# Optimization experiments

Measured on AMD Instinct MI355X. Metric: run time of the kernel, lower is better.

Reference implementation:

```python
import jax, jax.numpy as jnp
import numpy as np

EPS = 1e-5

def layernorm(x, w, b):
    mu = jnp.mean(x, axis=-1, keepdims=True)
    var = jnp.mean((x - mu) ** 2, axis=-1, keepdims=True)
    return (x - mu) / jnp.sqrt(var + EPS) * w + b

def setup_inputs() -> dict:
    key = jax.random.key(0)
    ks = jax.random.split(key, 20)
    N, E, G = 50000, 800000, 512
    IN, OUT, TXT, MAN = 128, 128, 768, 14
    d = {
        "x": jax.random.normal(ks[0], (N, IN), jnp.float32),
        "edge_index": jax.random.randint(ks[1], (2, E), 0, N),
        "batch": jnp.sort(jax.random.randint(ks[2], (N,), 0, G)),
        "batch_size": G,
        "text_embedding": jax.random.normal(ks[3], (G, TXT), jnp.float32),
        "features_embedding": jax.random.normal(ks[4], (G, MAN), jnp.float32),
        # params
        "ln_proj_w": jnp.ones((IN,)), "ln_proj_b": jnp.zeros((IN,)),
        "W_l": jax.random.normal(ks[5], (IN, OUT)) / np.sqrt(IN),
        "b_l": jnp.zeros((OUT,)),
        "W_r": jax.random.normal(ks[6], (IN, OUT)) / np.sqrt(IN),
        "ln_conv_w": jnp.ones((OUT,)), "ln_conv_b": jnp.zeros((OUT,)),
        "gate_w": jax.random.normal(ks[7], (OUT, 1)) / np.sqrt(OUT),
        "gate_b": jnp.zeros((1,)),
        "graph_weight": jnp.asarray(1.0, jnp.float32),
        "msg_W": jax.random.normal(ks[8], (TXT, OUT)) / np.sqrt(TXT),
        "msg_b": jnp.zeros((OUT,)),
        "feat_W": jax.random.normal(ks[9], (MAN, OUT)) / np.sqrt(MAN),
        "feat_b": jnp.zeros((OUT,)),
        "mixed_w": jnp.ones((3 * OUT,)), "mixed_b": jnp.zeros((3 * OUT,)),
        "fc1_W": jax.random.normal(ks[10], (3 * OUT, 1)) / np.sqrt(3 * OUT),
        "fc1_b": jnp.zeros((1,)),
    }
    return d

def reference(x, edge_index, batch, batch_size, text_embedding, features_embedding,
              ln_proj_w, ln_proj_b, W_l, b_l, W_r, ln_conv_w, ln_conv_b,
              gate_w, gate_b, graph_weight, msg_W, msg_b, feat_W, feat_b,
              mixed_w, mixed_b, fc1_W, fc1_b):
    N = x.shape[0]
    src, dst = edge_index[0], edge_index[1]
    # project_norm
    h = layernorm(x, ln_proj_w, ln_proj_b)
    # GraphSAGE (SAGEConv, mean aggregation): out = mean_j(h_j) @ W_l + b + h @ W_r
    msgs = h[src]                                   # [E, IN] gather
    agg = jax.ops.segment_sum(msgs, dst, num_segments=N)
    deg = jax.ops.segment_sum(jnp.ones((src.shape[0],), h.dtype), dst, num_segments=N)
    mean_nb = agg / jnp.maximum(deg, 1.0)[:, None]
    h = mean_nb @ W_l + b_l + h @ W_r
    # layernorm + gelu (HomogeneousGraphConvolution)
    h = jax.nn.gelu(layernorm(h, ln_conv_w, ln_conv_b), approximate=False)
    # AttentionalAggregation: scatter-softmax over `batch`
    gate = (h @ gate_w + gate_b)[:, 0]              # [N]
    seg_max = jax.ops.segment_max(gate, batch, num_segments=batch_size)
    seg_max = jnp.where(jnp.isfinite(seg_max), seg_max, 0.0)
    e = jnp.exp(gate - seg_max[batch])
    denom = jax.ops.segment_sum(e, batch, num_segments=batch_size)
    attn = (e / denom[batch])[:, None]              # [N,1]
    graph_embedding = jax.ops.segment_sum(attn * h, batch, num_segments=batch_size)
    # dropout is identity in eval mode
    weighted = graph_weight * graph_embedding
    msg_emb = jax.nn.gelu(text_embedding @ msg_W + msg_b, approximate=False)
    feat_emb = jax.nn.gelu(features_embedding @ feat_W + feat_b, approximate=False)
    emb = jnp.concatenate([weighted, msg_emb, feat_emb], axis=1)
    emb = layernorm(emb, mixed_w, mixed_b)
    logits = emb @ fc1_W + fc1_b
    return (logits, graph_embedding, attn)
```

## Files before the change

kernel.cpp:

```cpp
#include <hip/hip_runtime.h>


typedef unsigned short ushort_t;
typedef __attribute__((ext_vector_type(8))) short bf16x8;
typedef __attribute__((ext_vector_type(4))) float floatx4;

__device__ __forceinline__ float b2f(ushort_t u) {
    union { unsigned int i; float f; } v; v.i = ((unsigned int)u) << 16; return v.f;
}
__device__ __forceinline__ ushort_t f2b(float f) {
    union { float f; unsigned int i; } v; v.f = f;
    unsigned int x = v.i;
    return (ushort_t)((x + 0x7FFFu + ((x >> 16) & 1u)) >> 16);
}
__device__ __forceinline__ float gelu_f(float x) {
    return 0.5f * x * (1.0f + erff(x * 0.70710678118654752440f));
}
__device__ __forceinline__ float waveReduceSum(float v) {
#pragma unroll
    for (int o = 32; o; o >>= 1) v += __shfl_xor(v, o, 64);
    return v;
}
__device__ __forceinline__ int waveReduceSumI(int v) {
#pragma unroll
    for (int o = 32; o; o >>= 1) v += __shfl_xor(v, o, 64);
    return v;
}
__device__ __forceinline__ float waveReduceMax(float v) {
#pragma unroll
    for (int o = 32; o; o >>= 1) v = fmaxf(v, __shfl_xor(v, o, 64));
    return v;
}
__device__ __forceinline__ int lowerBound(const int* __restrict__ a, int n, int v) {
    int lo = 0, hi = n;
    while (lo < hi) { int mid = (lo + hi) >> 1; if (a[mid] < v) lo = mid + 1; else hi = mid; }
    return lo;
}

__global__ void __launch_bounds__(256) k_prepln(
    const float* __restrict__ x, const float* __restrict__ w, const float* __restrict__ b,
    const float* __restrict__ Wl, const float* __restrict__ Wr,
    ushort_t* __restrict__ Wt, ushort_t* __restrict__ hb, int* __restrict__ deg, int N) {
    int bid = blockIdx.x;
    if (bid < 128) {
        int id = bid * 256 + threadIdx.x;
        int n = id >> 8, k = id & 255;
        float v = (k < 128) ? Wl[k * 128 + n] : Wr[(k - 128) * 128 + n];
        Wt[n * 256 + k] = f2b(v);
        return;
    }
    int lb = bid - 128;
    if (threadIdx.x < 4) {
        int rz = lb * 4 + threadIdx.x;
        if (rz < N) deg[rz] = 0;
    }
    int row  = lb * 4 + (threadIdx.x >> 6);
    int lane = threadIdx.x & 63;
    if (row >= N) return;
    size_t base = (size_t)row * 128;
    float2 xv = ((const float2*)(x + base))[lane];
    float v0 = xv.x, v1 = xv.y;
    float s  = waveReduceSum(v0 + v1);
    float s2 = waveReduceSum(v0 * v0 + v1 * v1);
    float mu = s * (1.0f / 128.0f);
    float var = s2 * (1.0f / 128.0f) - mu * mu;
    float rstd = 1.0f / sqrtf(var + 1e-5f);
    int d = lane * 2;
    ushort2 ov;
    ov.x = f2b((v0 - mu) * rstd * w[d]     + b[d]);
    ov.y = f2b((v1 - mu) * rstd * w[d + 1] + b[d + 1]);
    ((ushort2*)(hb + base))[lane] = ov;
}

__global__ void __launch_bounds__(256) k_count(
    const int* __restrict__ ei, int* __restrict__ deg, int E) {
    int i0 = (blockIdx.x * 256 + threadIdx.x) * 4;
    const int* dstp = ei + E;
    if (i0 + 3 < E) {
        int4 d4 = *(const int4*)(dstp + i0);
        atomicAdd(&deg[d4.x], 1);
        atomicAdd(&deg[d4.y], 1);
        atomicAdd(&deg[d4.z], 1);
        atomicAdd(&deg[d4.w], 1);
    } else {
        int e1 = min(i0 + 4, E);
        for (int i = i0; i < e1; i++) atomicAdd(&deg[dstp[i]], 1);
    }
}

__global__ void __launch_bounds__(256) k_cursor3(
    const int* __restrict__ deg, int* __restrict__ cursor, int* __restrict__ wcur, int N) {
    int c = blockIdx.x, t = threadIdx.x;
    __shared__ int sb[256];
    __shared__ int cw[4];
    int lim = c << 8;
    int part = 0;
    for (int j = t; j < lim; j += 256) part += deg[j];
    part = waveReduceSumI(part);
    int lane = t & 63, wv = t >> 6;
    if (lane == 0) cw[wv] = part;
    int i = (c << 8) + t;
    int v = (i < N) ? deg[i] : 0;
    sb[t] = v;
    __syncthreads();
    for (int o = 1; o < 256; o <<= 1) {
        int a = (t >= o) ? sb[t - o] : 0;
        __syncthreads();
        sb[t] += a;
        __syncthreads();
    }
    int coff = cw[0] + cw[1] + cw[2] + cw[3];
    if (i < N) {
        int cv = sb[t] - v + coff;
        cursor[i] = cv;
        wcur[i]   = cv;
    }
}

__global__ void __launch_bounds__(256) k_place(
    const int* __restrict__ ei, int* __restrict__ wcur, int* __restrict__ nbr, int E) {
    int i0 = (blockIdx.x * 256 + threadIdx.x) * 4;
    if (i0 + 3 < E) {
        int4 s4 = *(const int4*)(ei + i0);
        int4 d4 = *(const int4*)(ei + E + i0);
        nbr[atomicAdd(&wcur[d4.x], 1)] = s4.x;
        nbr[atomicAdd(&wcur[d4.y], 1)] = s4.y;
        nbr[atomicAdd(&wcur[d4.z], 1)] = s4.z;
        nbr[atomicAdd(&wcur[d4.w], 1)] = s4.w;
    } else {
        int e1 = min(i0 + 4, E);
        for (int i = i0; i < e1; i++) {
            int s = ei[i], d = ei[E + i];
            nbr[atomicAdd(&wcur[d], 1)] = s;
        }
    }
}

__global__ void __launch_bounds__(256) k_aggemm(
    const ushort_t* __restrict__ hb, const ushort_t* __restrict__ Wt,
    const float* __restrict__ bl, const float* __restrict__ lnw,
    const float* __restrict__ lnb, const float* __restrict__ gw,
    const float* __restrict__ gb, const int* __restrict__ deg,
    const int* __restrict__ cursor, const int* __restrict__ nbr,
    ushort_t* __restrict__ h3b, float* __restrict__ gate, int N) {
    __shared__ ushort_t A[16][264];
    __shared__ float H2[16][132];
    int t = threadIdx.x;
    int row0 = blockIdx.x * 16;
    int w = t >> 6, l = t & 63;
    int sub = l >> 4, li = l & 15;
    for (int rr = 0; rr < 4; rr++) {
        int r = w * 4 + rr;
        int node = row0 + r; if (node >= N) node = N - 1;
        if (sub == 2) {
            bf16x8 hv = *(const bf16x8*)(hb + (size_t)node * 128 + li * 8);
            *(bf16x8*)&A[r][128 + li * 8] = hv;
        }
        int dg = deg[node];
        int st = cursor[node];
        float a0 = 0.f, a1 = 0.f, a2 = 0.f, a3 = 0.f;
        float a4 = 0.f, a5 = 0.f, a6 = 0.f, a7 = 0.f;
        for (int j = 0; j < dg; j += 8) {
            int i0 = j + sub, i1 = j + 4 + sub;
            bf16x8 r0 = {0,0,0,0,0,0,0,0};
            bf16x8 r1 = {0,0,0,0,0,0,0,0};
            if (i0 < dg) {
                int s = nbr[st + i0];
                r0 = *(const bf16x8*)(hb + (size_t)s * 128 + li * 8);
            }
            if (i1 < dg) {
                int s = nbr[st + i1];
                r1 = *(const bf16x8*)(hb + (size_t)s * 128 + li * 8);
            }
            a0 += b2f((ushort_t)r0[0]) + b2f((ushort_t)r1[0]);
            a1 += b2f((ushort_t)r0[1]) + b2f((ushort_t)r1[1]);
            a2 += b2f((ushort_t)r0[2]) + b2f((ushort_t)r1[2]);
            a3 += b2f((ushort_t)r0[3]) + b2f((ushort_t)r1[3]);
            a4 += b2f((ushort_t)r0[4]) + b2f((ushort_t)r1[4]);
            a5 += b2f((ushort_t)r0[5]) + b2f((ushort_t)r1[5]);
            a6 += b2f((ushort_t)r0[6]) + b2f((ushort_t)r1[6]);
            a7 += b2f((ushort_t)r0[7]) + b2f((ushort_t)r1[7]);
        }
        a0 += __shfl_xor(a0, 16, 64); a0 += __shfl_xor(a0, 32, 64);
        a1 += __shfl_xor(a1, 16, 64); a1 += __shfl_xor(a1, 32, 64);
        a2 += __shfl_xor(a2, 16, 64); a2 += __shfl_xor(a2, 32, 64);
        a3 += __shfl_xor(a3, 16, 64); a3 += __shfl_xor(a3, 32, 64);
        a4 += __shfl_xor(a4, 16, 64); a4 += __shfl_xor(a4, 32, 64);
        a5 += __shfl_xor(a5, 16, 64); a5 += __shfl_xor(a5, 32, 64);
        a6 += __shfl_xor(a6, 16, 64); a6 += __shfl_xor(a6, 32, 64);
        a7 += __shfl_xor(a7, 16, 64); a7 += __shfl_xor(a7, 32, 64);
        if (sub == 0) {
            float inv = 1.0f / fmaxf((float)dg, 1.0f);
            bf16x8 ov;
            ov[0] = (short)f2b(a0 * inv); ov[1] = (short)f2b(a1 * inv);
            ov[2] = (short)f2b(a2 * inv); ov[3] = (short)f2b(a3 * inv);
            ov[4] = (short)f2b(a4 * inv); ov[5] = (short)f2b(a5 * inv);
            ov[6] = (short)f2b(a6 * inv); ov[7] = (short)f2b(a7 * inv);
            *(bf16x8*)&A[r][li * 8] = ov;
        }
    }
    __syncthreads();
    int m16 = l & 15, quad = l >> 4;
    int n0 = w * 32 + m16;
    int n1 = n0 + 16;
    floatx4 acc0 = {0.f, 0.f, 0.f, 0.f}, acc1 = {0.f, 0.f, 0.f, 0.f};
    for (int ks = 0; ks < 256; ks += 32) {
        bf16x8 a  = *(const bf16x8*)&A[m16][ks + quad * 8];
        bf16x8 b0 = *(const bf16x8*)(Wt + (size_t)n0 * 256 + ks + quad * 8);
        bf16x8 b1 = *(const bf16x8*)(Wt + (size_t)n1 * 256 + ks + quad * 8);
        acc0 = __builtin_amdgcn_mfma_f32_16x16x32_bf16(a, b0, acc0, 0, 0, 0);
        acc1 = __builtin_amdgcn_mfma_f32_16x16x32_bf16(a, b1, acc1, 0, 0, 0);
    }
#pragma unroll
    for (int i = 0; i < 4; i++) {
        H2[quad * 4 + i][n0] = acc0[i];
        H2[quad * 4 + i][n1] = acc1[i];
    }
    __syncthreads();
    int d = l * 2;
    float bb0 = bl[d],  bb1 = bl[d + 1];
    float lw0 = lnw[d], lw1 = lnw[d + 1];
    float lb0 = lnb[d], lb1 = lnb[d + 1];
    float gw0 = gw[d],  gw1 = gw[d + 1];
    float gbias = gb[0];
#pragma unroll
    for (int rr = 0; rr < 4; rr++) {
        int r = w * 4 + rr;
        int row = row0 + r;
        if (row >= N) break;
        float v0 = H2[r][d] + bb0, v1 = H2[r][d + 1] + bb1;
        float s  = waveReduceSum(v0 + v1);
        float s2 = waveReduceSum(v0 * v0 + v1 * v1);
        float mu = s * (1.f / 128.f);
        float var = s2 * (1.f / 128.f) - mu * mu;
        float rstd = 1.0f / sqrtf(var + 1e-5f);
        float g0 = gelu_f((v0 - mu) * rstd * lw0 + lb0);
        float g1 = gelu_f((v1 - mu) * rstd * lw1 + lb1);
        float gp = waveReduceSum(g0 * gw0 + g1 * gw1);
        ushort2 ov; ov.x = f2b(g0); ov.y = f2b(g1);
        ((ushort2*)(h3b + (size_t)row * 128))[l] = ov;
        if (l == 0) gate[row] = gp + gbias;
    }
}

__global__ void __launch_bounds__(128) k_attntail(
    const float* __restrict__ gate, const ushort_t* __restrict__ h3b,
    const int* __restrict__ batch,
    const float* __restrict__ text, const float* __restrict__ feats,
    const float* __restrict__ msgW, const float* __restrict__ msgb,
    const float* __restrict__ featW, const float* __restrict__ featb,
    const float* __restrict__ gwt, const float* __restrict__ mixw,
    const float* __restrict__ mixb, const float* __restrict__ fc1W,
    const float* __restrict__ fc1b,
    float* __restrict__ ge_out, float* __restrict__ attn_out,
    float* __restrict__ logits, int N, int G) {
    int g = blockIdx.x, t = threadIdx.x;
    __shared__ int sbound[2];
    __shared__ float wbuf[2];
    __shared__ float pbuf[128];
    __shared__ float txt[768];
    __shared__ float rbuf[4];
    if (t < 2) sbound[t] = lowerBound(batch, N, g + t);
    for (int i = t; i < 768; i += 128) txt[i] = text[(size_t)g * 768 + i];
    __syncthreads();
    int s0 = sbound[0], s1 = sbound[1];
    int lane = t & 63, wv = t >> 6;
    float acc = 0.f;
    if (s1 > s0) {
        float m = -3.0e38f;
        for (int i = s0 + t; i < s1; i += 128) m = fmaxf(m, gate[i]);
        m = waveReduceMax(m);
        if (lane == 0) wbuf[wv] = m;
        __syncthreads();
        m = fmaxf(wbuf[0], wbuf[1]);
        __syncthreads();
        float dsum = 0.f;
        for (int i = s0 + t; i < s1; i += 128) dsum += expf(gate[i] - m);
        dsum = waveReduceSum(dsum);
        if (lane == 0) wbuf[wv] = dsum;
        __syncthreads();
        float inv = 1.0f / (wbuf[0] + wbuf[1]);
        for (int base = s0; base < s1; base += 128) {
            int n = min(128, s1 - base);
            __syncthreads();
            if (t < n) {
                float p = expf(gate[base + t] - m) * inv;
                pbuf[t] = p;
                attn_out[base + t] = p;
            }
            __syncthreads();
            for (int j = 0; j < n; j++)
                acc += pbuf[j] * b2f(h3b[(size_t)(base + j) * 128 + t]);
        }
    }
    ge_out[(size_t)g * 128 + t] = acc;
    float am = msgb[t];
    for (int k = 0; k < 768; k += 4) {
        float4 a = *(const float4*)&txt[k];
        am += a.x * msgW[(k + 0) * 128 + t] + a.y * msgW[(k + 1) * 128 + t]
            + a.z * msgW[(k + 2) * 128 + t] + a.w * msgW[(k + 3) * 128 + t];
    }
    float me = gelu_f(am);
    float af = featb[t];
#pragma unroll
    for (int k = 0; k < 14; k++) af += feats[g * 14 + k] * featW[k * 128 + t];
    float fe = gelu_f(af);
    float e0 = gwt[0] * acc;
    float ps = e0 + me + fe, ps2 = e0 * e0 + me * me + fe * fe;
    float r1 = waveReduceSum(ps), r2 = waveReduceSum(ps2);
    __syncthreads();
    if (lane == 0) { rbuf[wv] = r1; rbuf[2 + wv] = r2; }
    __syncthreads();
    float S = rbuf[0] + rbuf[1], S2 = rbuf[2] + rbuf[3];
    float mu = S * (1.f / 384.f);
    float var = S2 * (1.f / 384.f) - mu * mu;
    float rstd = 1.0f / sqrtf(var + 1e-5f);
    float n0 = (e0 - mu) * rstd * mixw[t]       + mixb[t];
    float n1 = (me - mu) * rstd * mixw[128 + t] + mixb[128 + t];
    float n2 = (fe - mu) * rstd * mixw[256 + t] + mixb[256 + t];
    float lp = n0 * fc1W[t] + n1 * fc1W[128 + t] + n2 * fc1W[256 + t];
    float r3 = waveReduceSum(lp);
    __syncthreads();
    if (lane == 0) rbuf[wv] = r3;
    __syncthreads();
    if (t == 0) logits[g] = rbuf[0] + rbuf[1] + fc1b[0];
}

extern "C" void kernel_launch(void* const* d_in, const int* in_sizes, int n_in,
                              void* d_out, int out_size, void* d_ws, size_t ws_size,
                              hipStream_t stream) {
    const float* x     = (const float*)d_in[0];
    const int*   ei    = (const int*)d_in[1];
    const int*   batch = (const int*)d_in[2];
    const float* text  = (const float*)d_in[4];
    const float* feats = (const float*)d_in[5];
    const float* lnpw  = (const float*)d_in[6];
    const float* lnpb  = (const float*)d_in[7];
    const float* Wl    = (const float*)d_in[8];
    const float* bl    = (const float*)d_in[9];
    const float* Wr    = (const float*)d_in[10];
    const float* lncw  = (const float*)d_in[11];
    const float* lncb  = (const float*)d_in[12];
    const float* gatew = (const float*)d_in[13];
    const float* gateb = (const float*)d_in[14];
    const float* gwt   = (const float*)d_in[15];
    const float* msgW  = (const float*)d_in[16];
    const float* msgb  = (const float*)d_in[17];
    const float* featW = (const float*)d_in[18];
    const float* featb = (const float*)d_in[19];
    const float* mixw  = (const float*)d_in[20];
    const float* mixb  = (const float*)d_in[21];
    const float* fc1W  = (const float*)d_in[22];
    const float* fc1b  = (const float*)d_in[23];

    int N = in_sizes[0] / 128;
    int E = in_sizes[1] / 2;
    int G = in_sizes[4] / 768;

    char* wp = (char*)d_ws;
    auto alloc = [&](size_t bytes) -> char* {
        char* p = wp; wp += (bytes + 255) & ~(size_t)255; return p;
    };
    ushort_t* hb     = (ushort_t*)alloc((size_t)N * 128 * 2);
    ushort_t* h3b    = (ushort_t*)alloc((size_t)N * 128 * 2);
    ushort_t* Wt     = (ushort_t*)alloc(128 * 256 * 2);
    float*    gate   = (float*)alloc((size_t)N * 4);
    int*      deg    = (int*)alloc((size_t)N * 4);
    int*      cursor = (int*)alloc((size_t)N * 4);
    int*      wcur   = (int*)alloc((size_t)N * 4);
    int*      nbr    = (int*)alloc((size_t)E * 4);

    int nch = (N + 255) / 256;
    int eb  = (E + 1023) / 1024;

    float* logits_out = (float*)d_out;
    float* ge_out     = logits_out + G;
    float* attn_out   = ge_out + (size_t)G * 128;

    k_prepln   <<<128 + (N + 3) / 4, 256, 0, stream>>>(x, lnpw, lnpb, Wl, Wr, Wt, hb, deg, N);
    k_count    <<<eb,                256, 0, stream>>>(ei, deg, E);
    k_cursor3  <<<nch,               256, 0, stream>>>(deg, cursor, wcur, N);
    k_place    <<<eb,                256, 0, stream>>>(ei, wcur, nbr, E);
    k_aggemm   <<<(N + 15) / 16,     256, 0, stream>>>(hb, Wt, bl, lncw, lncb, gatew, gateb,
                                                       deg, cursor, nbr, h3b, gate, N);
    k_attntail <<<G,                 128, 0, stream>>>(gate, h3b, batch, text, feats,
                                                       msgW, msgb, featW, featb, gwt,
                                                       mixw, mixb, fc1W, fc1b,
                                                       ge_out, attn_out, logits_out, N, G);
}
```

Measured before the change: 325.7 us.

## Assign one node per 16-lane group in neighbor aggregation with unrolled gathers

Restructures the mean-aggregation phase so that each 16-lane subgroup handles a whole node's neighbor list. Before, all four subgroups split the neighbors of one node and the wave looped over four nodes. Each lane now issues up to eight independent neighbor gathers per iteration, and the cross-subgroup shuffle reduction and the serial per-node loop are gone. This raises memory-level parallelism, but lanes within a wave now diverge when node degrees differ, and register use grows from the eight in-flight loads.

```diff
diff --git a/kernel.cpp b/kernel.cpp
--- a/kernel.cpp
+++ b/kernel.cpp
@@ -35,6 +35,12 @@
     int lo = 0, hi = n;
     while (lo < hi) { int mid = (lo + hi) >> 1; if (a[mid] < v) lo = mid + 1; else hi = mid; }
     return lo;
+}
+__device__ __forceinline__ void acc8(float* a, const bf16x8& r) {
+    a[0] += b2f((ushort_t)r[0]); a[1] += b2f((ushort_t)r[1]);
+    a[2] += b2f((ushort_t)r[2]); a[3] += b2f((ushort_t)r[3]);
+    a[4] += b2f((ushort_t)r[4]); a[5] += b2f((ushort_t)r[5]);
+    a[6] += b2f((ushort_t)r[6]); a[7] += b2f((ushort_t)r[7]);
 }
 
 __global__ void __launch_bounds__(256) k_prepln(
@@ -149,55 +155,52 @@
     int row0 = blockIdx.x * 16;
     int w = t >> 6, l = t & 63;
     int sub = l >> 4, li = l & 15;
-    for (int rr = 0; rr < 4; rr++) {
-        int r = w * 4 + rr;
+    {
+        int r = w * 4 + sub;
         int node = row0 + r; if (node >= N) node = N - 1;
-        if (sub == 2) {
-            bf16x8 hv = *(const bf16x8*)(hb + (size_t)node * 128 + li * 8);
-            *(bf16x8*)&A[r][128 + li * 8] = hv;
-        }
+        bf16x8 hv = *(const bf16x8*)(hb + (size_t)node * 128 + li * 8);
+        *(bf16x8*)&A[r][128 + li * 8] = hv;
         int dg = deg[node];
         int st = cursor[node];
-        float a0 = 0.f, a1 = 0.f, a2 = 0.f, a3 = 0.f;
-        float a4 = 0.f, a5 = 0.f, a6 = 0.f, a7 = 0.f;
-        for (int j = 0; j < dg; j += 8) {
-            int i0 = j + sub, i1 = j + 4 + sub;
-            bf16x8 r0 = {0,0,0,0,0,0,0,0};
-            bf16x8 r1 = {0,0,0,0,0,0,0,0};
-            if (i0 < dg) {
-                int s = nbr[st + i0];
-                r0 = *(const bf16x8*)(hb + (size_t)s * 128 + li * 8);
-            }
-            if (i1 < dg) {
-                int s = nbr[st + i1];
-                r1 = *(const bf16x8*)(hb + (size_t)s * 128 + li * 8);
-            }
-            a0 += b2f((ushort_t)r0[0]) + b2f((ushort_t)r1[0]);
-            a1 += b2f((ushort_t)r0[1]) + b2f((ushort_t)r1[1]);
-            a2 += b2f((ushort_t)r0[2]) + b2f((ushort_t)r1[2]);
-            a3 += b2f((ushort_t)r0[3]) + b2f((ushort_t)r1[3]);
-            a4 += b2f((ushort_t)r0[4]) + b2f((ushort_t)r1[4]);
-            a5 += b2f((ushort_t)r0[5]) + b2f((ushort_t)r1[5]);
-            a6 += b2f((ushort_t)r0[6]) + b2f((ushort_t)r1[6]);
-            a7 += b2f((ushort_t)r0[7]) + b2f((ushort_t)r1[7]);
-        }
-        a0 += __shfl_xor(a0, 16, 64); a0 += __shfl_xor(a0, 32, 64);
-        a1 += __shfl_xor(a1, 16, 64); a1 += __shfl_xor(a1, 32, 64);
-        a2 += __shfl_xor(a2, 16, 64); a2 += __shfl_xor(a2, 32, 64);
-        a3 += __shfl_xor(a3, 16, 64); a3 += __shfl_xor(a3, 32, 64);
-        a4 += __shfl_xor(a4, 16, 64); a4 += __shfl_xor(a4, 32, 64);
-        a5 += __shfl_xor(a5, 16, 64); a5 += __shfl_xor(a5, 32, 64);
-        a6 += __shfl_xor(a6, 16, 64); a6 += __shfl_xor(a6, 32, 64);
-        a7 += __shfl_xor(a7, 16, 64); a7 += __shfl_xor(a7, 32, 64);
-        if (sub == 0) {
-            float inv = 1.0f / fmaxf((float)dg, 1.0f);
-            bf16x8 ov;
-            ov[0] = (short)f2b(a0 * inv); ov[1] = (short)f2b(a1 * inv);
-            ov[2] = (short)f2b(a2 * inv); ov[3] = (short)f2b(a3 * inv);
-            ov[4] = (short)f2b(a4 * inv); ov[5] = (short)f2b(a5 * inv);
-            ov[6] = (short)f2b(a6 * inv); ov[7] = (short)f2b(a7 * inv);
-            *(bf16x8*)&A[r][li * 8] = ov;
-        }
+        float a[8] = {0.f, 0.f, 0.f, 0.f, 0.f, 0.f, 0.f, 0.f};
+        int j = 0;
+        for (; j + 8 <= dg; j += 8) {
+            int s0 = nbr[st + j],     s1 = nbr[st + j + 1];
+            int s2 = nbr[st + j + 2], s3 = nbr[st + j + 3];
+            int s4 = nbr[st + j + 4], s5 = nbr[st + j + 5];
+            int s6 = nbr[st + j + 6], s7 = nbr[st + j + 7];
+            bf16x8 r0 = *(const bf16x8*)(hb + (size_t)s0 * 128 + li * 8);
+            bf16x8 r1 = *(const bf16x8*)(hb + (size_t)s1 * 128 + li * 8);
+            bf16x8 r2 = *(const bf16x8*)(hb + (size_t)s2 * 128 + li * 8);
+            bf16x8 r3 = *(const bf16x8*)(hb + (size_t)s3 * 128 + li * 8);
+            bf16x8 r4 = *(const bf16x8*)(hb + (size_t)s4 * 128 + li * 8);
+            bf16x8 r5 = *(const bf16x8*)(hb + (size_t)s5 * 128 + li * 8);
+            bf16x8 r6 = *(const bf16x8*)(hb + (size_t)s6 * 128 + li * 8);
+            bf16x8 r7 = *(const bf16x8*)(hb + (size_t)s7 * 128 + li * 8);
+            acc8(a, r0); acc8(a, r1); acc8(a, r2); acc8(a, r3);
+            acc8(a, r4); acc8(a, r5); acc8(a, r6); acc8(a, r7);
+        }
+        for (; j + 4 <= dg; j += 4) {
+            int s0 = nbr[st + j],     s1 = nbr[st + j + 1];
+            int s2 = nbr[st + j + 2], s3 = nbr[st + j + 3];
+            bf16x8 r0 = *(const bf16x8*)(hb + (size_t)s0 * 128 + li * 8);
+            bf16x8 r1 = *(const bf16x8*)(hb + (size_t)s1 * 128 + li * 8);
+            bf16x8 r2 = *(const bf16x8*)(hb + (size_t)s2 * 128 + li * 8);
+            bf16x8 r3 = *(const bf16x8*)(hb + (size_t)s3 * 128 + li * 8);
+            acc8(a, r0); acc8(a, r1); acc8(a, r2); acc8(a, r3);
+        }
+        for (; j < dg; j++) {
+            int s = nbr[st + j];
+            bf16x8 r0 = *(const bf16x8*)(hb + (size_t)s * 128 + li * 8);
+            acc8(a, r0);
+        }
+        float inv = 1.0f / fmaxf((float)dg, 1.0f);
+        bf16x8 ov;
+        ov[0] = (short)f2b(a[0] * inv); ov[1] = (short)f2b(a[1] * inv);
+        ov[2] = (short)f2b(a[2] * inv); ov[3] = (short)f2b(a[3] * inv);
+        ov[4] = (short)f2b(a[4] * inv); ov[5] = (short)f2b(a[5] * inv);
+        ov[6] = (short)f2b(a[6] * inv); ov[7] = (short)f2b(a[7] * inv);
+        *(bf16x8*)&A[r][li * 8] = ov;
     }
     __syncthreads();
     int m16 = l & 15, quad = l >> 4;
```

Result: faster. 316.8 us (-2.7%).
